# Performance work log

Hardware: AMD Instinct MI355X
Metric: run time of the kernel (lower is better)

The kernel has to match this reference:

```python
import jax, jax.numpy as jnp
import numpy as np

N_NODES = 156
NFEAT = 256
NHID = 128
B = 16384
T = 24
HLSTM = 32
ALPHA = 0.2


def setup_inputs() -> dict:
    key = jax.random.key(0)
    ks = jax.random.split(key, 16)
    f32 = jnp.float32
    inp = {
        "embedding": jax.random.normal(ks[0], (N_NODES, NFEAT), f32),
        "x": jax.random.normal(ks[1], (B, T, N_NODES), f32),
        "adj": jax.random.randint(ks[2], (N_NODES, N_NODES), 0, 2, jnp.int32),
        # GAT params (xavier-ish scale)
        "W_recent": jax.random.normal(ks[3], (NFEAT, NHID), f32) * 0.08,
        "a_recent": jax.random.normal(ks[4], (2 * NHID, 1), f32) * 0.1,
        "W_period": jax.random.normal(ks[5], (NFEAT, NHID), f32) * 0.08,
        "a_period": jax.random.normal(ks[6], (2 * NHID, 1), f32) * 0.1,
        # LSTM params, torch layout: weight_ih [4H, D], weight_hh [4H, H]
        "Wih_r": jax.random.normal(ks[7], (4 * HLSTM, N_NODES), f32) * 0.08,
        "Whh_r": jax.random.normal(ks[8], (4 * HLSTM, HLSTM), f32) * 0.08,
        "bih_r": jnp.zeros((4 * HLSTM,), f32),
        "bhh_r": jnp.zeros((4 * HLSTM,), f32),
        "Wih_p": jax.random.normal(ks[9], (4 * HLSTM, N_NODES), f32) * 0.08,
        "Whh_p": jax.random.normal(ks[10], (4 * HLSTM, HLSTM), f32) * 0.08,
        "bih_p": jnp.zeros((4 * HLSTM,), f32),
        "bhh_p": jnp.zeros((4 * HLSTM,), f32),
        "fc_W": jax.random.normal(ks[11], (N_NODES, 2 * HLSTM), f32) * 0.1,
        "fc_b": jnp.zeros((N_NODES,), f32),
    }
    return inp


def _gat_attention(embedding, W, a, adj):
    # h = embedding @ W : [N, F]
    h = embedding @ W
    F = h.shape[1]
    # e[i,j] = leakyrelu(h_i . a[:F] + h_j . a[F:])  (same math as the
    # repeat/cat construction, without materializing [N*N, 2F])
    s1 = h @ a[:F, 0]   # [N]
    s2 = h @ a[F:, 0]   # [N]
    e = jax.nn.leaky_relu(s1[:, None] + s2[None, :], ALPHA)
    e = jnp.where(adj > 0, e, jnp.float32(-9e15))
    return jax.nn.softmax(e, axis=1)  # [N, N]


def _lstm_last(x_seq, Wih, Whh, bih, bhh):
    # x_seq: [B, T, D]; returns last hidden state [B, H]
    H = Whh.shape[1]
    Bn = x_seq.shape[0]
    h0 = jnp.zeros((Bn, H), x_seq.dtype)
    c0 = jnp.zeros((Bn, H), x_seq.dtype)
    bias = bih + bhh

    def step(carry, xt):
        h, c = carry
        g = xt @ Wih.T + h @ Whh.T + bias
        i, f, gg, o = jnp.split(g, 4, axis=-1)  # torch gate order i,f,g,o
        c = jax.nn.sigmoid(f) * c + jax.nn.sigmoid(i) * jnp.tanh(gg)
        h = jax.nn.sigmoid(o) * jnp.tanh(c)
        return (h, c), None

    (h, c), _ = jax.lax.scan(step, (h0, c0), jnp.swapaxes(x_seq, 0, 1))
    return h


def reference(embedding, x, adj, W_recent, a_recent, W_period, a_period,
              Wih_r, Whh_r, bih_r, bhh_r, Wih_p, Whh_p, bih_p, bhh_p,
              fc_W, fc_b):
    recent = x[:, :4, :]   # [B, 4, N]
    period = x[:, 4:, :]   # [B, T-4, N]

    # attention depends only on embedding/adj -> identical across timesteps
    attn_r = _gat_attention(embedding, W_recent, a_recent, adj)  # [N, N]
    attn_p = _gat_attention(embedding, W_period, a_period, adj)

    # out[b,t,i] = sum_j attn[i,j] * x[b,t,j]
    xr = jnp.einsum('ij,btj->bti', attn_r, recent)
    xp = jnp.einsum('ij,btj->bti', attn_p, period)

    hr = _lstm_last(xr, Wih_r, Whh_r, bih_r, bhh_r)  # [B, 32]
    hp = _lstm_last(xp, Wih_p, Whh_p, bih_p, bhh_p)  # [B, 32]

    h = jnp.concatenate([hr, hp], axis=1)            # [B, 64]
    return h @ fc_W.T + fc_b                         # [B, 156]
```

## Files before the change

kernel.cpp:

```cpp
#include <hip/hip_runtime.h>
#include <math.h>

#define N_NODES 156
#define NFEAT 256
#define NHID 128
#define BATCH 16384
#define TT 24
#define HLSTM 32
#define G4 128
#define ALPHA 0.2f

typedef __attribute__((ext_vector_type(8))) short bf16x8;
typedef __attribute__((ext_vector_type(4))) float f32x4;

static __device__ __forceinline__ unsigned short f2bf(float f) {
    unsigned u = __float_as_uint(f);
    u += 0x7fffu + ((u >> 16) & 1u);
    return (unsigned short)(u >> 16);
}
static __device__ __forceinline__ unsigned pk2(float lo, float hi) {
    return (unsigned)f2bf(lo) | ((unsigned)f2bf(hi) << 16);
}
static __device__ __forceinline__ bf16x8 cvt8(float4 a, float4 b) {
    bf16x8 r;
    r[0] = (short)f2bf(a.x); r[1] = (short)f2bf(a.y);
    r[2] = (short)f2bf(a.z); r[3] = (short)f2bf(a.w);
    r[4] = (short)f2bf(b.x); r[5] = (short)f2bf(b.y);
    r[6] = (short)f2bf(b.z); r[7] = (short)f2bf(b.w);
    return r;
}
static __device__ __forceinline__ float sigm(float x) { return 1.f / (1.f + __expf(-x)); }
static __device__ __forceinline__ float tanh_(float x) { return 1.f - 2.f / (__expf(2.f * x) + 1.f); }

__global__ void k_gat_s(const float* __restrict__ emb,
                        const float* __restrict__ Wr, const float* __restrict__ ar,
                        const float* __restrict__ Wp, const float* __restrict__ ap,
                        float* __restrict__ s_buf ) {
    int i = blockIdx.x;
    int gat = blockIdx.y;
    const float* W = gat ? Wp : Wr;
    const float* a = gat ? ap : ar;
    int j = threadIdx.x;
    __shared__ float erow[NFEAT];
    __shared__ float red[128];
    for (int k = j; k < NFEAT; k += 128) erow[k] = emb[i*NFEAT + k];
    __syncthreads();
    float h = 0.f;
    for (int k = 0; k < NFEAT; ++k) h = fmaf(erow[k], W[k*NHID + j], h);
    float v1 = h * a[j];
    float v2 = h * a[NHID + j];
    red[j] = v1; __syncthreads();
    for (int s = 64; s > 0; s >>= 1) { if (j < s) red[j] += red[j+s]; __syncthreads(); }
    if (j == 0) s_buf[(gat*2+0)*N_NODES + i] = red[0];
    __syncthreads();
    red[j] = v2; __syncthreads();
    for (int s = 64; s > 0; s >>= 1) { if (j < s) red[j] += red[j+s]; __syncthreads(); }
    if (j == 0) s_buf[(gat*2+1)*N_NODES + i] = red[0];
}

__global__ void k_attn(const float* __restrict__ s_buf, const int* __restrict__ adj,
                       float* __restrict__ attn ) {
    int i = blockIdx.x, gat = blockIdx.y;
    int j = threadIdx.x;
    __shared__ float red[256];
    float s1 = s_buf[(gat*2+0)*N_NODES + i];
    bool act = (j < N_NODES);
    float e = -INFINITY;
    if (act) {
        float s2 = s_buf[(gat*2+1)*N_NODES + j];
        float z = s1 + s2;
        z = (z > 0.f) ? z : ALPHA * z;
        if (adj[i*N_NODES + j] <= 0) z = -9e15f;
        e = z;
    }
    red[j] = e; __syncthreads();
    for (int s = 128; s > 0; s >>= 1) { if (j < s) red[j] = fmaxf(red[j], red[j+s]); __syncthreads(); }
    float m = red[0]; __syncthreads();
    float val = act ? __expf(e - m) : 0.f;
    red[j] = val; __syncthreads();
    for (int s = 128; s > 0; s >>= 1) { if (j < s) red[j] += red[j+s]; __syncthreads(); }
    float inv = 1.f / red[0];
    if (act) attn[(gat*N_NODES + i)*N_NODES + j] = val * inv;
}

__global__ void k_prep(const float* __restrict__ attn,
                       const float* __restrict__ Wih_r, const float* __restrict__ Wih_p,
                       const float* __restrict__ Whh_r, const float* __restrict__ Whh_p,
                       const float* __restrict__ bih_r, const float* __restrict__ bhh_r,
                       const float* __restrict__ bih_p, const float* __restrict__ bhh_p,
                       unsigned short* __restrict__ Mbf ,
                       unsigned short* __restrict__ Whhbf ,
                       float* __restrict__ bias2 ) {
    int g = blockIdx.x, gat = blockIdx.y;
    const float* Wih = gat ? Wih_p : Wih_r;
    const float* A = attn + gat*N_NODES*N_NODES;
    int j = threadIdx.x;
    if (j < 160) {
        float acc = 0.f;
        if (j < N_NODES)
            for (int n = 0; n < N_NODES; ++n)
                acc = fmaf(Wih[g*N_NODES + n], A[n*N_NODES + j], acc);
        Mbf[(gat*G4 + g)*160 + j] = f2bf(acc);
    }
    if (j < HLSTM)
        Whhbf[(gat*G4 + g)*HLSTM + j] = f2bf((gat ? Whh_p : Whh_r)[g*HLSTM + j]);
    if (g == 0 && j < G4)
        bias2[gat*G4 + j] = gat ? (bih_p[j] + bhh_p[j]) : (bih_r[j] + bhh_r[j]);
}

#define XS_HALF (64*160)
__global__ void __launch_bounds__(256, 1)
k_fused(const float* __restrict__ x,
        const unsigned short* __restrict__ Mbf,
        const unsigned short* __restrict__ Whhbf,
        const float* __restrict__ bias2,
        const float* __restrict__ fcW,
        const float* __restrict__ fcb,
        float* __restrict__ out) {
    __shared__ __align__(16) unsigned short xs[2*XS_HALF];
    __shared__ __align__(16) unsigned short hs[64*40];
    __shared__ __align__(16) unsigned short hcat[64*72];

    const int tid = threadIdx.x;
    const int w  = tid >> 6;
    const int l  = tid & 63;
    const int lm = l & 15;
    const int lg = l >> 4;
    const int brow = tid >> 2;
    const int q    = tid & 3;
    const int nf   = (q == 3) ? 9 : 10;
    const int b0 = blockIdx.x * 64;

    bf16x8 bfr[8][5];
    bf16x8 wrec[8];
    float  bias_v[8];
    float  cst[8];

#define LOAD_FRAGS(Mb, Wb, bs) do {                                          \
    _Pragma("unroll")                                                        \
    for (int nt = 0; nt < 8; ++nt) {                                         \
        int n_ = nt*16 + lm;                                                 \
        _Pragma("unroll")                                                    \
        for (int kf = 0; kf < 5; ++kf)                                       \
            bfr[nt][kf] = *(const bf16x8*)((Mb) + n_*160 + kf*32 + lg*8);    \
        wrec[nt]   = *(const bf16x8*)((Wb) + n_*HLSTM + lg*8);               \
        bias_v[nt] = (bs)[n_];                                               \
    } } while (0)

    if (q == 3) {
        *(uint2*)(xs + 0*XS_HALF + brow*160 + 156) = make_uint2(0u, 0u);
        *(uint2*)(xs + 1*XS_HALF + brow*160 + 156) = make_uint2(0u, 0u);
    }
    #pragma unroll
    for (int ds = 0; ds < 2; ++ds)
        #pragma unroll
        for (int i = 0; i < 4; ++i) {
            hs[(16*w + lg*4 + i)*40 + lm + 16*ds] = 0;
            cst[ds*4 + i] = 0.f;
        }
    LOAD_FRAGS(Mbf, Whhbf, bias2);

    float4 st[10];
    {
        const float* gp = x + ((size_t)(b0 + brow)*TT + 0)*N_NODES + q*40;
        #pragma unroll
        for (int i = 0; i < 10; ++i) if (i < nf) st[i] = ((const float4*)gp)[i];
        unsigned short* xw = xs + 0*XS_HALF + brow*160 + q*40;
        #pragma unroll
        for (int i = 0; i < 10; ++i) if (i < nf) {
            uint2 p; p.x = pk2(st[i].x, st[i].y); p.y = pk2(st[i].z, st[i].w);
            *(uint2*)(xw + i*4) = p;
        }
    }

    #pragma unroll 2
    for (int t = 0; t < TT; ++t) {
        const int cur = t & 1;
        if (t < TT-1) {
            const float* gp = x + ((size_t)(b0 + brow)*TT + (t+1))*N_NODES + q*40;
            #pragma unroll
            for (int i = 0; i < 10; ++i) if (i < nf) st[i] = ((const float4*)gp)[i];
        }

        f32x4 acc[8];
        #pragma unroll
        for (int nt = 0; nt < 8; ++nt) acc[nt] = (f32x4){0.f, 0.f, 0.f, 0.f};
        #pragma unroll
        for (int kf = 0; kf < 5; ++kf) {
            bf16x8 af = *(const bf16x8*)(xs + cur*XS_HALF + (16*w + lm)*160 + kf*32 + lg*8);
            #pragma unroll
            for (int nt = 0; nt < 8; ++nt)
                acc[nt] = __builtin_amdgcn_mfma_f32_16x16x32_bf16(af, bfr[nt][kf], acc[nt], 0, 0, 0);
        }
        {
            bf16x8 hf = *(const bf16x8*)(hs + (16*w + lm)*40 + lg*8);
            #pragma unroll
            for (int nt = 0; nt < 8; ++nt)
                acc[nt] = __builtin_amdgcn_mfma_f32_16x16x32_bf16(hf, wrec[nt], acc[nt], 0, 0, 0);
        }

        #pragma unroll
        for (int ds = 0; ds < 2; ++ds)
            #pragma unroll
            for (int i = 0; i < 4; ++i) {
                float gi = acc[0 + ds][i] + bias_v[0 + ds];
                float gf = acc[2 + ds][i] + bias_v[2 + ds];
                float gg = acc[4 + ds][i] + bias_v[4 + ds];
                float go = acc[6 + ds][i] + bias_v[6 + ds];
                float si = sigm(gi), sf = sigm(gf), so = sigm(go);
                float c  = sf * cst[ds*4 + i] + si * tanh_(gg);
                float h  = so * tanh_(c);
                int r = 16*w + lg*4 + i;
                int d = lm + 16*ds;
                if (t == 3) {
                    hcat[r*72 + d] = f2bf(h);
                    hs[r*40 + d]   = 0;
                    cst[ds*4 + i]  = 0.f;
                } else {
                    cst[ds*4 + i] = c;
                    hs[r*40 + d]  = f2bf(h);
                    if (t == TT-1) hcat[r*72 + 32 + d] = f2bf(h);
                }
            }

        if (t == 3)
            LOAD_FRAGS(Mbf + G4*160, Whhbf + G4*HLSTM, bias2 + G4);

        if (t < TT-1) {
            unsigned short* xw = xs + (cur ^ 1)*XS_HALF + brow*160 + q*40;
            #pragma unroll
            for (int i = 0; i < 10; ++i) if (i < nf) {
                uint2 p; p.x = pk2(st[i].x, st[i].y); p.y = pk2(st[i].z, st[i].w);
                *(uint2*)(xw + i*4) = p;
            }
        }
    }

    {
        bf16x8 ha0 = *(const bf16x8*)(hcat + (16*w + lm)*72 + lg*8);
        bf16x8 ha1 = *(const bf16x8*)(hcat + (16*w + lm)*72 + 32 + lg*8);
        #pragma unroll
        for (int nt = 0; nt < 10; ++nt) {
            int n  = nt*16 + lm;
            int nc = n < 155 ? n : 155;
            const float* wp0 = fcW + nc*64 + lg*8;
            const float* wp1 = fcW + nc*64 + 32 + lg*8;
            bf16x8 wf0 = cvt8(*(const float4*)wp0, *(const float4*)(wp0 + 4));
            bf16x8 wf1 = cvt8(*(const float4*)wp1, *(const float4*)(wp1 + 4));
            f32x4 fa = (f32x4){0.f, 0.f, 0.f, 0.f};
            fa = __builtin_amdgcn_mfma_f32_16x16x32_bf16(ha0, wf0, fa, 0, 0, 0);
            fa = __builtin_amdgcn_mfma_f32_16x16x32_bf16(ha1, wf1, fa, 0, 0, 0);
            if (n < N_NODES) {
                float bn = fcb[n];
                #pragma unroll
                for (int i = 0; i < 4; ++i)
                    out[(size_t)(b0 + 16*w + lg*4 + i)*N_NODES + n] = fa[i] + bn;
            }
        }
    }
#undef LOAD_FRAGS
}

extern "C" void kernel_launch(void* const* d_in, const int* in_sizes, int n_in,
                              void* d_out, int out_size, void* d_ws, size_t ws_size,
                              hipStream_t stream) {
    (void)in_sizes; (void)n_in; (void)out_size; (void)ws_size;
    const float* emb   = (const float*)d_in[0];
    const float* x     = (const float*)d_in[1];
    const int*   adj   = (const int*)d_in[2];
    const float* Wr    = (const float*)d_in[3];
    const float* ar    = (const float*)d_in[4];
    const float* Wp    = (const float*)d_in[5];
    const float* ap    = (const float*)d_in[6];
    const float* Wih_r = (const float*)d_in[7];
    const float* Whh_r = (const float*)d_in[8];
    const float* bih_r = (const float*)d_in[9];
    const float* bhh_r = (const float*)d_in[10];
    const float* Wih_p = (const float*)d_in[11];
    const float* Whh_p = (const float*)d_in[12];
    const float* bih_p = (const float*)d_in[13];
    const float* bhh_p = (const float*)d_in[14];
    const float* fcW   = (const float*)d_in[15];
    const float* fcb   = (const float*)d_in[16];
    float* out = (float*)d_out;

    char* ws = (char*)d_ws;
    size_t off = 0;
    auto alloc = [&](size_t bytes) {
        char* p = ws + off;
        off += (bytes + 255) & ~(size_t)255;
        return p;
    };
    float*          attn  = (float*)alloc(2*156*156*sizeof(float));
    float*          sbuf  = (float*)alloc(4*156*sizeof(float));
    unsigned short* Mbf   = (unsigned short*)alloc(2*G4*160*sizeof(unsigned short));
    unsigned short* Whhbf = (unsigned short*)alloc(2*G4*HLSTM*sizeof(unsigned short));
    float*          bias2 = (float*)alloc(2*G4*sizeof(float));

    k_gat_s<<<dim3(156, 2), 128, 0, stream>>>(emb, Wr, ar, Wp, ap, sbuf);
    k_attn<<<dim3(156, 2), 256, 0, stream>>>(sbuf, adj, attn);
    k_prep<<<dim3(128, 2), 192, 0, stream>>>(attn, Wih_r, Wih_p, Whh_r, Whh_p,
                                             bih_r, bhh_r, bih_p, bhh_p,
                                             Mbf, Whhbf, bias2);
    k_fused<<<dim3(256), 256, 0, stream>>>(x, Mbf, Whhbf, bias2, fcW, fcb, out);
}
```

Before: 111.1 us.

## Prefetch x two steps ahead in fragment layout with smaller blocks

Each wave now loads its own 16 batch rows of x directly in MFMA A-fragment order and keeps two register buffers, so global loads run two timesteps ahead of the compute. The blocks shrink from 4 waves/64 rows to 2 waves/32 rows, which gives 512 blocks and better spreading across CUs. Bias is folded into the accumulator init, and the conversion now uses the hip bf16 intrinsics. The costs are more register pressure from the two prefetch buffers and a less coalesced, strided load pattern.

Measured after the change: 97.62 us. -12.1%, faster.

```diff
diff --git a/kernel.cpp b/kernel.cpp
--- a/kernel.cpp
+++ b/kernel.cpp
@@ -1,4 +1,5 @@
 #include <hip/hip_runtime.h>
+#include <hip/hip_bf16.h>
 #include <math.h>
 
 #define N_NODES 156
@@ -9,6 +10,8 @@
 #define HLSTM 32
 #define G4 128
 #define ALPHA 0.2f
+#define NW 2
+#define ROWS_B (NW*16)
 
 typedef __attribute__((ext_vector_type(8))) short bf16x8;
 typedef __attribute__((ext_vector_type(4))) float f32x4;
@@ -18,16 +21,13 @@
     u += 0x7fffu + ((u >> 16) & 1u);
     return (unsigned short)(u >> 16);
 }
-static __device__ __forceinline__ unsigned pk2(float lo, float hi) {
-    return (unsigned)f2bf(lo) | ((unsigned)f2bf(hi) << 16);
-}
-static __device__ __forceinline__ bf16x8 cvt8(float4 a, float4 b) {
-    bf16x8 r;
-    r[0] = (short)f2bf(a.x); r[1] = (short)f2bf(a.y);
-    r[2] = (short)f2bf(a.z); r[3] = (short)f2bf(a.w);
-    r[4] = (short)f2bf(b.x); r[5] = (short)f2bf(b.y);
-    r[6] = (short)f2bf(b.z); r[7] = (short)f2bf(b.w);
-    return r;
+static __device__ __forceinline__ bf16x8 cv8(float4 a, float4 b) {
+    union { __hip_bfloat16 h[8]; bf16x8 v; } u;
+    u.h[0] = __float2bfloat16(a.x); u.h[1] = __float2bfloat16(a.y);
+    u.h[2] = __float2bfloat16(a.z); u.h[3] = __float2bfloat16(a.w);
+    u.h[4] = __float2bfloat16(b.x); u.h[5] = __float2bfloat16(b.y);
+    u.h[6] = __float2bfloat16(b.z); u.h[7] = __float2bfloat16(b.w);
+    return u.v;
 }
 static __device__ __forceinline__ float sigm(float x) { return 1.f / (1.f + __expf(-x)); }
 static __device__ __forceinline__ float tanh_(float x) { return 1.f - 2.f / (__expf(2.f * x) + 1.f); }
@@ -108,8 +108,9 @@
         bias2[gat*G4 + j] = gat ? (bih_p[j] + bhh_p[j]) : (bih_r[j] + bhh_r[j]);
 }
 
-#define XS_HALF (64*160)
-__global__ void __launch_bounds__(256, 1)
+#define XS_W (5*64*8)
+#define XS_B (NW*XS_W)
+__global__ void __launch_bounds__(NW*64, 1)
 k_fused(const float* __restrict__ x,
         const unsigned short* __restrict__ Mbf,
         const unsigned short* __restrict__ Whhbf,
@@ -117,19 +118,17 @@
         const float* __restrict__ fcW,
         const float* __restrict__ fcb,
         float* __restrict__ out) {
-    __shared__ __align__(16) unsigned short xs[2*XS_HALF];
-    __shared__ __align__(16) unsigned short hs[64*40];
-    __shared__ __align__(16) unsigned short hcat[64*72];
+    __shared__ __align__(16) unsigned short xs[2*XS_B];
+    __shared__ __align__(16) unsigned short hfrag[NW*512];
+    __shared__ __align__(16) unsigned short hcatf[NW*1024];
 
     const int tid = threadIdx.x;
     const int w  = tid >> 6;
     const int l  = tid & 63;
     const int lm = l & 15;
     const int lg = l >> 4;
-    const int brow = tid >> 2;
-    const int q    = tid & 3;
-    const int nf   = (q == 3) ? 9 : 10;
-    const int b0 = blockIdx.x * 64;
+    const int b0 = blockIdx.x * ROWS_B;
+    const size_t xrow = (size_t)(b0 + 16*w + lm) * (TT*N_NODES);
 
     bf16x8 bfr[8][5];
     bf16x8 wrec[8];
@@ -147,106 +146,98 @@
         bias_v[nt] = (bs)[n_];                                               \
     } } while (0)
 
-    if (q == 3) {
-        *(uint2*)(xs + 0*XS_HALF + brow*160 + 156) = make_uint2(0u, 0u);
-        *(uint2*)(xs + 1*XS_HALF + brow*160 + 156) = make_uint2(0u, 0u);
-    }
     #pragma unroll
     for (int ds = 0; ds < 2; ++ds)
         #pragma unroll
         for (int i = 0; i < 4; ++i) {
-            hs[(16*w + lg*4 + i)*40 + lm + 16*ds] = 0;
+            hfrag[w*512 + ((lm>>3) + 2*ds)*128 + (lg*4 + i)*8 + (lm&7)] = 0;
             cst[ds*4 + i] = 0.f;
         }
     LOAD_FRAGS(Mbf, Whhbf, bias2);
 
-    float4 st[10];
+    float4 fA[10], fB[10];
+    const float4 f4z = make_float4(0.f, 0.f, 0.f, 0.f);
+
+#define ISSUE(F, TL) do {                                                    \
+    const float* bp_ = x + xrow + (size_t)(TL)*N_NODES + lg*8;               \
+    _Pragma("unroll")                                                        \
+    for (int kf = 0; kf < 5; ++kf) {                                         \
+        F[2*kf]   = *(const float4*)(bp_ + kf*32);                           \
+        F[2*kf+1] = (kf == 4 && lg == 3) ? f4z                               \
+                                         : *(const float4*)(bp_ + kf*32 + 4);\
+    } } while (0)
+
+#define CVTW(F, NB) do {                                                     \
+    unsigned short* xw_ = xs + (NB)*XS_B + w*XS_W + l*8;                     \
+    _Pragma("unroll")                                                        \
+    for (int kf = 0; kf < 5; ++kf)                                           \
+        *(bf16x8*)(xw_ + kf*512) = cv8(F[2*kf], F[2*kf+1]);                  \
+    } while (0)
+
+    ISSUE(fA, 0);
+    ISSUE(fB, 1);
+    CVTW(fA, 0);
+
+#define STEP(T_, FC, FN) do {                                                \
+    if ((T_) + 2 < TT) ISSUE(FN, (T_) + 2);                                  \
+    if ((T_) + 1 < TT) CVTW(FC, ((T_) + 1) & 1);       \
+    f32x4 acc[8];                                                            \
+    _Pragma("unroll")                                                        \
+    for (int nt = 0; nt < 8; ++nt)                                           \
+        acc[nt] = (f32x4){bias_v[nt], bias_v[nt], bias_v[nt], bias_v[nt]};   \
+    { const unsigned short* xr_ = xs + ((T_)&1)*XS_B + w*XS_W + l*8;         \
+      _Pragma("unroll")                                                      \
+      for (int kf = 0; kf < 5; ++kf) {                                       \
+          bf16x8 af = *(const bf16x8*)(xr_ + kf*512);                        \
+          _Pragma("unroll")                                                  \
+          for (int nt = 0; nt < 8; ++nt)                                     \
+              acc[nt] = __builtin_amdgcn_mfma_f32_16x16x32_bf16(af, bfr[nt][kf], acc[nt], 0, 0, 0); \
+      }                                                                      \
+      bf16x8 hf = *(const bf16x8*)(hfrag + w*512 + l*8);                     \
+      _Pragma("unroll")                                                      \
+      for (int nt = 0; nt < 8; ++nt)                                         \
+          acc[nt] = __builtin_amdgcn_mfma_f32_16x16x32_bf16(hf, wrec[nt], acc[nt], 0, 0, 0); \
+    }                                                                        \
+    _Pragma("unroll")                                                        \
+    for (int ds = 0; ds < 2; ++ds)                                           \
+        _Pragma("unroll")                                                    \
+        for (int i = 0; i < 4; ++i) {                                        \
+            float si = sigm(acc[0 + ds][i]);                                 \
+            float sf = sigm(acc[2 + ds][i]);                                 \
+            float tg = tanh_(acc[4 + ds][i]);                                \
+            float so = sigm(acc[6 + ds][i]);                                 \
+            float c  = sf * cst[ds*4 + i] + si * tg;                         \
+            float h  = so * tanh_(c);                                        \
+            int cidx = ((lm>>3) + 2*ds)*128 + (lg*4 + i)*8 + (lm&7);         \
+            if ((T_) == 3) {               \
+                hcatf[w*1024 + cidx] = f2bf(h);                              \
+                hfrag[w*512 + cidx]  = 0;                                    \
+                cst[ds*4 + i] = 0.f;                                         \
+            } else {                                                         \
+                cst[ds*4 + i] = c;                                           \
+                hfrag[w*512 + cidx] = f2bf(h);                               \
+                if ((T_) == TT-1) hcatf[w*1024 + 512 + cidx] = f2bf(h);      \
+            }                                                                \
+        }                                                                    \
+    if ((T_) == 3) LOAD_FRAGS(Mbf + G4*160, Whhbf + G4*HLSTM, bias2 + G4);   \
+    } while (0)
+
+    for (int t = 0; t < TT; t += 2) {
+        STEP(t,     fB, fA);
+        STEP(t + 1, fA, fB);
+    }
+
     {
-        const float* gp = x + ((size_t)(b0 + brow)*TT + 0)*N_NODES + q*40;
-        #pragma unroll
-        for (int i = 0; i < 10; ++i) if (i < nf) st[i] = ((const float4*)gp)[i];
-        unsigned short* xw = xs + 0*XS_HALF + brow*160 + q*40;
-        #pragma unroll
-        for (int i = 0; i < 10; ++i) if (i < nf) {
-            uint2 p; p.x = pk2(st[i].x, st[i].y); p.y = pk2(st[i].z, st[i].w);
-            *(uint2*)(xw + i*4) = p;
-        }
-    }
-
-    #pragma unroll 2
-    for (int t = 0; t < TT; ++t) {
-        const int cur = t & 1;
-        if (t < TT-1) {
-            const float* gp = x + ((size_t)(b0 + brow)*TT + (t+1))*N_NODES + q*40;
-            #pragma unroll
-            for (int i = 0; i < 10; ++i) if (i < nf) st[i] = ((const float4*)gp)[i];
-        }
-
-        f32x4 acc[8];
-        #pragma unroll
-        for (int nt = 0; nt < 8; ++nt) acc[nt] = (f32x4){0.f, 0.f, 0.f, 0.f};
-        #pragma unroll
-        for (int kf = 0; kf < 5; ++kf) {
-            bf16x8 af = *(const bf16x8*)(xs + cur*XS_HALF + (16*w + lm)*160 + kf*32 + lg*8);
-            #pragma unroll
-            for (int nt = 0; nt < 8; ++nt)
-                acc[nt] = __builtin_amdgcn_mfma_f32_16x16x32_bf16(af, bfr[nt][kf], acc[nt], 0, 0, 0);
-        }
-        {
-            bf16x8 hf = *(const bf16x8*)(hs + (16*w + lm)*40 + lg*8);
-            #pragma unroll
-            for (int nt = 0; nt < 8; ++nt)
-                acc[nt] = __builtin_amdgcn_mfma_f32_16x16x32_bf16(hf, wrec[nt], acc[nt], 0, 0, 0);
-        }
-
-        #pragma unroll
-        for (int ds = 0; ds < 2; ++ds)
-            #pragma unroll
-            for (int i = 0; i < 4; ++i) {
-                float gi = acc[0 + ds][i] + bias_v[0 + ds];
-                float gf = acc[2 + ds][i] + bias_v[2 + ds];
-                float gg = acc[4 + ds][i] + bias_v[4 + ds];
-                float go = acc[6 + ds][i] + bias_v[6 + ds];
-                float si = sigm(gi), sf = sigm(gf), so = sigm(go);
-                float c  = sf * cst[ds*4 + i] + si * tanh_(gg);
-                float h  = so * tanh_(c);
-                int r = 16*w + lg*4 + i;
-                int d = lm + 16*ds;
-                if (t == 3) {
-                    hcat[r*72 + d] = f2bf(h);
-                    hs[r*40 + d]   = 0;
-                    cst[ds*4 + i]  = 0.f;
-                } else {
-                    cst[ds*4 + i] = c;
-                    hs[r*40 + d]  = f2bf(h);
-                    if (t == TT-1) hcat[r*72 + 32 + d] = f2bf(h);
-                }
-            }
-
-        if (t == 3)
-            LOAD_FRAGS(Mbf + G4*160, Whhbf + G4*HLSTM, bias2 + G4);
-
-        if (t < TT-1) {
-            unsigned short* xw = xs + (cur ^ 1)*XS_HALF + brow*160 + q*40;
-            #pragma unroll
-            for (int i = 0; i < 10; ++i) if (i < nf) {
-                uint2 p; p.x = pk2(st[i].x, st[i].y); p.y = pk2(st[i].z, st[i].w);
-                *(uint2*)(xw + i*4) = p;
-            }
-        }
-    }
-
-    {
-        bf16x8 ha0 = *(const bf16x8*)(hcat + (16*w + lm)*72 + lg*8);
-        bf16x8 ha1 = *(const bf16x8*)(hcat + (16*w + lm)*72 + 32 + lg*8);
+        bf16x8 ha0 = *(const bf16x8*)(hcatf + w*1024 + l*8);
+        bf16x8 ha1 = *(const bf16x8*)(hcatf + w*1024 + 512 + l*8);
         #pragma unroll
         for (int nt = 0; nt < 10; ++nt) {
             int n  = nt*16 + lm;
             int nc = n < 155 ? n : 155;
             const float* wp0 = fcW + nc*64 + lg*8;
             const float* wp1 = fcW + nc*64 + 32 + lg*8;
-            bf16x8 wf0 = cvt8(*(const float4*)wp0, *(const float4*)(wp0 + 4));
-            bf16x8 wf1 = cvt8(*(const float4*)wp1, *(const float4*)(wp1 + 4));
+            bf16x8 wf0 = cv8(*(const float4*)wp0, *(const float4*)(wp0 + 4));
+            bf16x8 wf1 = cv8(*(const float4*)wp1, *(const float4*)(wp1 + 4));
             f32x4 fa = (f32x4){0.f, 0.f, 0.f, 0.f};
             fa = __builtin_amdgcn_mfma_f32_16x16x32_bf16(ha0, wf0, fa, 0, 0, 0);
             fa = __builtin_amdgcn_mfma_f32_16x16x32_bf16(ha1, wf1, fa, 0, 0, 0);
@@ -258,6 +249,9 @@
             }
         }
     }
+#undef STEP
+#undef CVTW
+#undef ISSUE
 #undef LOAD_FRAGS
 }
 
@@ -302,5 +296,5 @@
     k_prep<<<dim3(128, 2), 192, 0, stream>>>(attn, Wih_r, Wih_p, Whh_r, Whh_p,
                                              bih_r, bhh_r, bih_p, bhh_p,
                                              Mbf, Whhbf, bias2);
-    k_fused<<<dim3(256), 256, 0, stream>>>(x, Mbf, Whhbf, bias2, fcW, fcb, out);
-}
+    k_fused<<<dim3(BATCH/ROWS_B), NW*64, 0, stream>>>(x, Mbf, Whhbf, bias2, fcW, fcb, out);
+}
```
